# Optimization experiments

Hardware: AMD Instinct MI355X
Metric: run time of the kernel (lower is better)

Reference implementation:

```python
import jax, jax.numpy as jnp
import numpy as np
import math

B, S, D, H, L, V = 16, 512, 1024, 16, 128, 32000
DH = D // H


def _posenc(s, d):
    pos = np.arange(s, dtype=np.float32)[:, None]
    div = np.exp(np.arange(0, d, 2, dtype=np.float32) * (-math.log(10000.0) / d))
    pe = np.zeros((s, d), dtype=np.float32)
    pe[:, 0::2] = np.sin(pos * div)
    pe[:, 1::2] = np.cos(pos * div)
    return jnp.asarray(pe)


def _ln(x, g, b):
    m = jnp.mean(x, axis=-1, keepdims=True)
    v = jnp.mean((x - m) ** 2, axis=-1, keepdims=True)
    return (x - m) / jnp.sqrt(v + 1e-5) * g + b


def setup_inputs():
    key = jax.random.key(0)
    ks = jax.random.split(key, 16)
    w = lambda k, *sh: 0.02 * jax.random.normal(k, sh, dtype=jnp.float32)
    return {
        'x': jax.random.randint(ks[0], (B, S), 0, V),
        'embed': w(ks[1], V, D),
        'Wq': w(ks[2], D, D), 'bq': jnp.zeros((D,), jnp.float32),
        'Wk': w(ks[3], D, D), 'bk': jnp.zeros((D,), jnp.float32),
        'Wv': w(ks[4], D, D), 'bv': jnp.zeros((D,), jnp.float32),
        'Wo': w(ks[5], D, D), 'bo': jnp.zeros((D,), jnp.float32),
        'g1': jnp.ones((D,), jnp.float32), 'be1': jnp.zeros((D,), jnp.float32),
        'W1': w(ks[6], D, D), 'bf1': jnp.zeros((D,), jnp.float32),
        'W2': w(ks[7], D, D), 'bf2': jnp.zeros((D,), jnp.float32),
        'g2': jnp.ones((D,), jnp.float32), 'be2': jnp.zeros((D,), jnp.float32),
        'g3': jnp.ones((D,), jnp.float32), 'be3': jnp.zeros((D,), jnp.float32),
        'Wmu': w(ks[8], D, L), 'bmu': jnp.zeros((L,), jnp.float32),
        'Wsig': w(ks[9], D, L), 'bsig': jnp.zeros((L,), jnp.float32),
        'eps': jax.random.normal(ks[10], (B, S, L), dtype=jnp.float32),
    }


def reference(x, embed, Wq, bq, Wk, bk, Wv, bv, Wo, bo, g1, be1, W1, bf1, W2, bf2,
              g2, be2, g3, be3, Wmu, bmu, Wsig, bsig, eps):
    h = embed[x] * jnp.asarray(D ** 0.5, jnp.float32)          # [B,S,D]
    h = h + _posenc(S, D)                                       # dropout = identity (eval)
    h = _ln(h, g1, be1)
    # attention (faithful to source: raw reshape head-split, scale = dh/2)
    Q = (h @ Wq + bq).reshape(B, H, S, DH)
    K = (h @ Wk + bk).reshape(B, H, S, DH)
    Vv = (h @ Wv + bv).reshape(B, H, S, DH)
    scores = jnp.einsum('bhqd,bhkd->bhqk', Q, K) / (DH / 2.0)
    attn = jax.nn.softmax(scores, axis=-1)
    ctx = jnp.einsum('bhqk,bhkd->bhqd', attn, Vv).reshape(B, S, D)
    ctx = ctx @ Wo + bo
    h = h + ctx
    h = _ln(h, g2, be2)
    f = jax.nn.leaky_relu(h @ W1 + bf1, 0.01) @ W2 + bf2
    h = f + f                                                    # source: x = ffn(x); x = x + drop2(x)
    h = _ln(h, g3, be3)
    mu = h @ Wmu + bmu
    sigma = jnp.exp(h @ Wsig + bsig)
    z = mu + sigma * eps
    return z
```

## Files before the change

### kernel.cpp

```cpp
#include <hip/hip_runtime.h>
#include <cstdint>


typedef __bf16 bf16;
typedef __bf16 bf16x8 __attribute__((ext_vector_type(8)));
typedef __bf16 bf16x4 __attribute__((ext_vector_type(4)));
typedef float f32x4 __attribute__((ext_vector_type(4)));

#define MFMA16(a, b, c) __builtin_amdgcn_mfma_f32_16x16x32_bf16((a), (b), (c), 0, 0, 0)

#if __has_builtin(__builtin_amdgcn_exp2f)
#define EXP2F(x) __builtin_amdgcn_exp2f(x)
#else
#define EXP2F(x) exp2f(x)
#endif

__device__ __forceinline__ void async16(const bf16* g, bf16* l) {
  __builtin_amdgcn_global_load_lds(
      (const __attribute__((address_space(1))) unsigned int*)g,
      (__attribute__((address_space(3))) unsigned int*)l, 16, 0, 0);
}

#define VMWAIT(N)                                        \
  do {                                                   \
    asm volatile("s_waitcnt vmcnt(" #N ")" ::: "memory"); \
    __builtin_amdgcn_sched_barrier(0);                   \
  } while (0)
#define BAR() __builtin_amdgcn_s_barrier()

struct TP8 {
  const float* src[8];
  bf16* dst[8];
  int ncol[8];
};
__global__ __launch_bounds__(256) void transpose8_kernel(TP8 p) {
  const int z = blockIdx.z;
  const int N = p.ncol[z];
  const int tk = blockIdx.x * 64, tn = blockIdx.y * 64;
  if (tn >= N) return;
  const float* __restrict__ W = p.src[z];
  bf16* __restrict__ Wt = p.dst[z];
  __shared__ float tile[64][65];
  const int a = threadIdx.x >> 6, b = threadIdx.x & 63;
#pragma unroll
  for (int i = 0; i < 16; ++i) {
    int k = a + i * 4;
    tile[k][b] = W[(size_t)(tk + k) * N + tn + b];
  }
  __syncthreads();
#pragma unroll
  for (int i = 0; i < 16; ++i) {
    int n = a + i * 4;
    Wt[(size_t)(tn + n) * 1024 + tk + b] = (bf16)tile[b][n];
  }
}

__global__ __launch_bounds__(256) void embed_ln_kernel(const int* __restrict__ x,
                                                       const float* __restrict__ emb,
                                                       const float* __restrict__ g,
                                                       const float* __restrict__ be,
                                                       bf16* __restrict__ obf) {
  const int w = threadIdx.x >> 6, lane = threadIdx.x & 63;
  const int row = blockIdx.x * 4 + w;
  const int s = row & 511;
  const int t = x[row];
  const int c0 = lane * 16;
  const float* er = emb + (size_t)t * 1024 + c0;
  float o[16];
#pragma unroll
  for (int i = 0; i < 4; ++i) {
    const float4 e = *(const float4*)(er + i * 4);
    o[i * 4 + 0] = e.x; o[i * 4 + 1] = e.y; o[i * 4 + 2] = e.z; o[i * 4 + 3] = e.w;
  }
#pragma unroll
  for (int p = 0; p < 8; ++p) {
    const int cc = c0 + 2 * p;
    const float freq = __expf((float)cc * (-9.210340371976184f / 1024.0f));
    const float ang = (float)s * freq;
    o[2 * p] = o[2 * p] * 32.0f + __sinf(ang);
    o[2 * p + 1] = o[2 * p + 1] * 32.0f + __cosf(ang);
  }
  float sm = 0.f, q = 0.f;
#pragma unroll
  for (int j = 0; j < 16; ++j) { sm += o[j]; q += o[j] * o[j]; }
#pragma unroll
  for (int off = 1; off < 64; off <<= 1) {
    sm += __shfl_xor(sm, off);
    q += __shfl_xor(q, off);
  }
  const float mean = sm * (1.0f / 1024.0f);
  const float var = q * (1.0f / 1024.0f) - mean * mean;
  const float rstd = rsqrtf(var + 1e-5f);
  bf16 ob[16];
#pragma unroll
  for (int i = 0; i < 4; ++i) {
    const float4 gv = *(const float4*)(g + c0 + i * 4);
    const float4 bv = *(const float4*)(be + c0 + i * 4);
    const float gvv[4] = {gv.x, gv.y, gv.z, gv.w};
    const float bvv[4] = {bv.x, bv.y, bv.z, bv.w};
#pragma unroll
    for (int j = 0; j < 4; ++j)
      ob[i * 4 + j] = (bf16)((o[i * 4 + j] - mean) * rstd * gvv[j] + bvv[j]);
  }
  bf16* dst = obf + (size_t)row * 1024 + c0;
  *(uint4*)dst = *(const uint4*)&ob[0];
  *(uint4*)(dst + 8) = *(const uint4*)&ob[8];
}

__global__ __launch_bounds__(256) void ln_kernel(const bf16* __restrict__ in,
                                                 const float* __restrict__ g,
                                                 const float* __restrict__ be,
                                                 bf16* __restrict__ obf) {
  const int w = threadIdx.x >> 6, lane = threadIdx.x & 63;
  const int row = blockIdx.x * 4 + w;
  const int c0 = lane * 16;
  const bf16* src = in + (size_t)row * 1024 + c0;
  const bf16x8 v0 = *(const bf16x8*)src;
  const bf16x8 v1 = *(const bf16x8*)(src + 8);
  float v[16];
#pragma unroll
  for (int j = 0; j < 8; ++j) { v[j] = (float)v0[j]; v[8 + j] = (float)v1[j]; }
  float s = 0.f, q = 0.f;
#pragma unroll
  for (int j = 0; j < 16; ++j) { s += v[j]; q += v[j] * v[j]; }
#pragma unroll
  for (int off = 1; off < 64; off <<= 1) {
    s += __shfl_xor(s, off);
    q += __shfl_xor(q, off);
  }
  const float mean = s * (1.0f / 1024.0f);
  const float var = q * (1.0f / 1024.0f) - mean * mean;
  const float rstd = rsqrtf(var + 1e-5f);
  bf16 ob[16];
#pragma unroll
  for (int i = 0; i < 4; ++i) {
    const float4 gv = *(const float4*)(g + c0 + i * 4);
    const float4 bv = *(const float4*)(be + c0 + i * 4);
    const float gvv[4] = {gv.x, gv.y, gv.z, gv.w};
    const float bvv[4] = {bv.x, bv.y, bv.z, bv.w};
#pragma unroll
    for (int j = 0; j < 4; ++j)
      ob[i * 4 + j] = (bf16)((v[i * 4 + j] - mean) * rstd * gvv[j] + bvv[j]);
  }
  bf16* dst = obf + (size_t)row * 1024 + c0;
  *(uint4*)dst = *(const uint4*)&ob[0];
  *(uint4*)(dst + 8) = *(const uint4*)&ob[8];
}

__device__ __forceinline__ void ld_frags2(const bf16* sm, int rbase, int l15,
                                          int quad, bf16x8 out[2][2]) {
#pragma unroll
  for (int f = 0; f < 2; ++f) {
    const int row = rbase + f * 16 + l15;
    const int rx = row & 7;
#pragma unroll
    for (int h = 0; h < 2; ++h) {
      const int c = (h * 4 + quad) ^ rx;
      out[f][h] = *(const bf16x8*)(sm + (row * 8 + c) * 8);
    }
  }
}

template <int MQ, int NQ>
__device__ __forceinline__ void mma8(const bf16x8 aF[2][2], const bf16x8 bF[2][2],
                                     f32x4 acc[4][4]) {
  __builtin_amdgcn_s_setprio(1);
#pragma unroll
  for (int h = 0; h < 2; ++h)
#pragma unroll
    for (int m2 = 0; m2 < 2; ++m2)
#pragma unroll
      for (int n2 = 0; n2 < 2; ++n2)
        acc[MQ * 2 + m2][NQ * 2 + n2] =
            MFMA16(aF[m2][h], bF[n2][h], acc[MQ * 2 + m2][NQ * 2 + n2]);
  __builtin_amdgcn_s_setprio(0);
}

template <int MODE>
__global__ __launch_bounds__(512, 2) void gemm8_kernel(
    const bf16* __restrict__ A, const bf16* __restrict__ Bt,
    const float* __restrict__ b0f, const float* __restrict__ b1f,
    const float* __restrict__ b2f,
    bf16* __restrict__ o0, bf16* __restrict__ o1, bf16* __restrict__ o2,
    const bf16* __restrict__ residb,
    int M, int N, int K) {
  (void)M;
  __shared__ __attribute__((aligned(16))) bf16 Asm[2][128 * 64];
  __shared__ __attribute__((aligned(16))) bf16 Bsm[2][256 * 64];
  const int tid = threadIdx.x;
  const int wv = tid >> 6, lane = tid & 63;
  const int quad = lane >> 4, l15 = lane & 15;
  const int wm = wv & 1, wn = wv >> 1;
  const int m0 = blockIdx.x * 128, n0 = blockIdx.y * 256;

  f32x4 acc[4][4];
#pragma unroll
  for (int i = 0; i < 4; ++i)
#pragma unroll
    for (int j = 0; j < 4; ++j) acc[i][j] = {0.f, 0.f, 0.f, 0.f};

  size_t aoff[2], boff[2];
  int slds[2];
#pragma unroll
  for (int i = 0; i < 2; ++i) {
    const int s = tid + i * 512;
    const int r = s >> 3, c = (s & 7) ^ (r & 7);
    aoff[i] = (size_t)(m0 + r) * K + c * 8;
    boff[i] = (size_t)(n0 + r) * K + c * 8;
    slds[i] = s * 8;
  }
  auto stageA = [&](int buf, int t) {
#pragma unroll
    for (int i = 0; i < 2; ++i) async16(A + aoff[i] + t * 64, &Asm[buf][slds[i]]);
  };
  auto stageB = [&](int buf, int hh, int t) {
    const size_t ho = (size_t)hh * 128 * K;
    const int hl = hh * 8192;
#pragma unroll
    for (int i = 0; i < 2; ++i)
      async16(Bt + boff[i] + ho + t * 64, &Bsm[buf][hl + slds[i]]);
  };

  stageB(0, 0, 0); stageB(0, 1, 0); stageA(0, 0);
  stageB(1, 0, 1); stageB(1, 1, 1); stageA(1, 1);
  VMWAIT(6);
  BAR();

  bf16x8 aF[2][2], bF0[2][2], bF1[2][2];
  const int am0 = wm * 64, bn0 = wn * 64;

  auto phases = [&](int ne, int no, bool hn) {
    ld_frags2(&Asm[0][0], am0, l15, quad, aF);
    ld_frags2(&Bsm[0][0], bn0, l15, quad, bF0);
    BAR();
    mma8<0, 0>(aF, bF0, acc);
    BAR();
    ld_frags2(&Bsm[0][0], bn0 + 32, l15, quad, bF1);
    BAR();
    mma8<0, 1>(aF, bF1, acc);
    BAR();
    ld_frags2(&Asm[0][0], am0 + 32, l15, quad, aF);
    if (hn) stageB(0, 0, ne);
    BAR();
    mma8<1, 1>(aF, bF1, acc);
    BAR();
    if (hn) stageB(0, 1, ne);
    BAR();
    mma8<1, 0>(aF, bF0, acc);
    if (hn) { VMWAIT(4); } else { VMWAIT(0); }
    BAR();
    ld_frags2(&Asm[1][0], am0, l15, quad, aF);
    ld_frags2(&Bsm[1][0], bn0, l15, quad, bF0);
    if (hn) stageA(0, ne);
    BAR();
    mma8<0, 0>(aF, bF0, acc);
    BAR();
    ld_frags2(&Bsm[1][0], bn0 + 32, l15, quad, bF1);
    BAR();
    mma8<0, 1>(aF, bF1, acc);
    BAR();
    ld_frags2(&Asm[1][0], am0 + 32, l15, quad, aF);
    if (hn) stageB(1, 0, no);
    BAR();
    mma8<1, 1>(aF, bF1, acc);
    BAR();
    if (hn) { stageB(1, 1, no); stageA(1, no); }
    BAR();
    mma8<1, 0>(aF, bF0, acc);
    if (hn) { VMWAIT(6); }
    BAR();
  };

  const int nIter = K >> 7;
  for (int it = 0; it + 1 < nIter; ++it) phases(2 * it + 2, 2 * it + 3, true);
  phases(0, 0, false);

  const int part = (MODE == 6) ? ((int)blockIdx.y >> 2) : 0;
  bf16* ob = o0;
  const float* bp = b0f;
  if constexpr (MODE == 6) {
    ob = (part == 0) ? o0 : (part == 1 ? o1 : o2);
    bp = (part == 0) ? b0f : (part == 1 ? b1f : b2f);
  }
#pragma unroll
  for (int ni = 0; ni < 4; ++ni) {
    const int col = n0 + wn * 64 + ni * 16 + l15;
    const int cl = (MODE == 6) ? (col - part * 1024) : col;
    const float bv = bp[cl];
#pragma unroll
    for (int mi = 0; mi < 4; ++mi) {
#pragma unroll
      for (int r = 0; r < 4; ++r) {
        const int row = m0 + wm * 64 + mi * 16 + quad * 4 + r;
        float v = acc[mi][ni][r] + bv;
        if constexpr (MODE == 1) {
          const size_t idx = (size_t)row * N + col;
          o0[idx] = (bf16)(v + (float)residb[idx]);
        } else if constexpr (MODE == 2) {
          o0[(size_t)row * N + col] = (bf16)(v > 0.f ? v : 0.01f * v);
        } else if constexpr (MODE == 3) {
          o0[(size_t)row * N + col] = (bf16)(2.0f * v);
        } else {
          ob[(size_t)row * 1024 + cl] = (bf16)v;
        }
      }
    }
  }
}

__global__ __launch_bounds__(256) void gemm_musig(const bf16* __restrict__ A,
                                                  const bf16* __restrict__ Bt,
                                                  const float* __restrict__ bmu,
                                                  const float* __restrict__ bsig,
                                                  float* __restrict__ of) {
  constexpr int BK = 64;
  __shared__ __attribute__((aligned(16))) bf16 Asm[2][64 * BK];
  __shared__ __attribute__((aligned(16))) bf16 Bsm[2][128 * BK];
  const int tid = threadIdx.x;
  const int wv = tid >> 6, lane = tid & 63;
  const int quad = lane >> 4, l15 = lane & 15;
  const int m0 = blockIdx.x * 64, n0 = blockIdx.y * 128;
  const int wm = wv & 1, wn = wv >> 1;

  f32x4 acc[2][4];
#pragma unroll
  for (int i = 0; i < 2; ++i)
#pragma unroll
    for (int j = 0; j < 4; ++j) acc[i][j] = {0.f, 0.f, 0.f, 0.f};

  const bf16* Aglb[2];
  int asoff[2];
#pragma unroll
  for (int i = 0; i < 2; ++i) {
    const int s = tid + i * 256;
    const int row = s >> 3, col = (s & 7) ^ (row & 7);
    Aglb[i] = A + (size_t)(m0 + row) * 1024 + col * 8;
    asoff[i] = s * 8;
  }
  const bf16* Bglb[4];
  int bsoff[4];
#pragma unroll
  for (int i = 0; i < 4; ++i) {
    const int s = tid + i * 256;
    const int row = s >> 3, col = (s & 7) ^ (row & 7);
    Bglb[i] = Bt + (size_t)(n0 + row) * 1024 + col * 8;
    bsoff[i] = s * 8;
  }

#pragma unroll
  for (int i = 0; i < 2; ++i) async16(Aglb[i], &Asm[0][asoff[i]]);
#pragma unroll
  for (int i = 0; i < 4; ++i) async16(Bglb[i], &Bsm[0][bsoff[i]]);
  __syncthreads();

  for (int k = 0; k < 16; ++k) {
    const int cur = k & 1, nxt = cur ^ 1;
    bf16x8 af[2][2], bfr[4][2];
#pragma unroll
    for (int mi = 0; mi < 2; ++mi) {
      const int row = wm * 32 + mi * 16 + l15;
#pragma unroll
      for (int h = 0; h < 2; ++h) {
        const int pos = (h * 4 + quad) ^ (row & 7);
        af[mi][h] = *(const bf16x8*)(&Asm[cur][(row * 8 + pos) * 8]);
      }
    }
#pragma unroll
    for (int ni = 0; ni < 4; ++ni) {
      const int row = wn * 64 + ni * 16 + l15;
#pragma unroll
      for (int h = 0; h < 2; ++h) {
        const int pos = (h * 4 + quad) ^ (row & 7);
        bfr[ni][h] = *(const bf16x8*)(&Bsm[cur][(row * 8 + pos) * 8]);
      }
    }
    if (k + 1 < 16) {
      const int ko = (k + 1) * BK;
#pragma unroll
      for (int i = 0; i < 2; ++i) async16(Aglb[i] + ko, &Asm[nxt][asoff[i]]);
#pragma unroll
      for (int i = 0; i < 4; ++i) async16(Bglb[i] + ko, &Bsm[nxt][bsoff[i]]);
    }
#pragma unroll
    for (int h = 0; h < 2; ++h)
#pragma unroll
      for (int mi = 0; mi < 2; ++mi)
#pragma unroll
        for (int ni = 0; ni < 4; ++ni)
          acc[mi][ni] = MFMA16(af[mi][h], bfr[ni][h], acc[mi][ni]);
    __syncthreads();
  }

#pragma unroll
  for (int ni = 0; ni < 4; ++ni) {
    const int col = n0 + wn * 64 + ni * 16 + l15;
    const float bv = (col < 128) ? bmu[col] : bsig[col - 128];
#pragma unroll
    for (int mi = 0; mi < 2; ++mi) {
#pragma unroll
      for (int r = 0; r < 4; ++r) {
        const int row = m0 + wm * 32 + mi * 16 + quad * 4 + r;
        of[(size_t)row * 256 + col] = acc[mi][ni][r] + bv;
      }
    }
  }
}

__global__ __launch_bounds__(256) void vtrans_kernel(const bf16* __restrict__ Vb,
                                                     bf16* __restrict__ VtG) {
  __shared__ float t[64][65];
  const int bh = blockIdx.x, kt = blockIdx.y;
  const int tid = threadIdx.x;
  const bf16* src = Vb + (size_t)bh * 32768 + (size_t)kt * 4096;
#pragma unroll
  for (int i = 0; i < 2; ++i) {
    int s = i * 256 + tid;
    int r = s >> 3, c = (s & 7) * 8;
    bf16x8 v = *(const bf16x8*)(src + (size_t)s * 8);
#pragma unroll
    for (int j = 0; j < 8; ++j) t[r][c + j] = (float)v[j];
  }
  __syncthreads();
  bf16* dst = VtG + (size_t)bh * 32768 + kt * 64;
#pragma unroll
  for (int i = 0; i < 2; ++i) {
    int s = i * 256 + tid;
    int d = s >> 3, kc = (s & 7) * 8;
    bf16 tmp[8];
#pragma unroll
    for (int j = 0; j < 8; ++j) tmp[j] = (bf16)t[kc + j][d];
    *(uint4*)(dst + (size_t)d * 512 + kc) = *(const uint4*)tmp;
  }
}

__global__ __launch_bounds__(256) void attn_kernel(const bf16* __restrict__ Qg,
                                                   const bf16* __restrict__ Kg,
                                                   const bf16* __restrict__ Vt,
                                                   bf16* __restrict__ ctx) {
  __shared__ __attribute__((aligned(16))) bf16 Ksm[128 * 64];
  __shared__ __attribute__((aligned(16))) bf16 Vsm[64 * 128];
  __shared__ __attribute__((aligned(16))) bf16 Psm[4][16 * 128];
  const int tid = threadIdx.x;
  const int w = tid >> 6, lane = tid & 63;
  const int quad = lane >> 4, l15 = lane & 15;
  const int bh = blockIdx.x;
  const size_t base = (size_t)bh * 32768;
  const bf16* Vth = Vt + base;
  const int qbase = blockIdx.y * 128 + w * 32;
  const f32x4 fz = {0.f, 0.f, 0.f, 0.f};

  bf16x8 a[2][2];
#pragma unroll
  for (int qt = 0; qt < 2; ++qt)
#pragma unroll
    for (int hf = 0; hf < 2; ++hf) {
      bf16x8 tq = *(const bf16x8*)(Qg + base +
                   (size_t)(qbase + qt * 16 + l15) * 64 + hf * 32 + quad * 8);
#pragma unroll
      for (int e = 0; e < 8; ++e) tq[e] = (bf16)((float)tq[e] * 0.045111758f);
      a[qt][hf] = tq;
    }

  f32x4 o[2][4];
  float l_i[2][4];
#pragma unroll
  for (int qt = 0; qt < 2; ++qt)
#pragma unroll
    for (int i = 0; i < 4; ++i) { o[qt][i] = fz; l_i[qt][i] = 0.f; }

  for (int kv0 = 0; kv0 < 512; kv0 += 128) {
#pragma unroll
    for (int i = 0; i < 4; ++i) {
      int s = i * 256 + tid;
      int r = s >> 3, c = (s & 7) ^ (r & 7);
      async16(Kg + base + (size_t)(kv0 + r) * 64 + c * 8, &Ksm[s * 8]);
    }
#pragma unroll
    for (int i = 0; i < 4; ++i) {
      int s = i * 256 + tid;
      int d = s >> 4, cs = s & 15;
      int c = (cs & 8) | ((cs & 7) ^ (d & 7));
      async16(Vth + (size_t)d * 512 + kv0 + c * 8, &Vsm[s * 8]);
    }
    __syncthreads();

    f32x4 sc[2][8];
#pragma unroll
    for (int j = 0; j < 8; ++j) {
      const int n = j * 16 + l15;
      const bf16x8 k0 = *(const bf16x8*)(&Ksm[(n * 8 + (quad ^ (n & 7))) * 8]);
      const bf16x8 k1 = *(const bf16x8*)(&Ksm[(n * 8 + ((4 + quad) ^ (n & 7))) * 8]);
      sc[0][j] = MFMA16(a[0][0], k0, fz);
      sc[0][j] = MFMA16(a[0][1], k1, sc[0][j]);
      sc[1][j] = MFMA16(a[1][0], k0, fz);
      sc[1][j] = MFMA16(a[1][1], k1, sc[1][j]);
    }

    bf16* ps = &Psm[w][0];
#pragma unroll
    for (int qt = 0; qt < 2; ++qt) {
#pragma unroll
      for (int r = 0; r < 4; ++r) {
        const int prow = quad * 4 + r;
        float sum = 0.f;
#pragma unroll
        for (int j = 0; j < 8; ++j) {
          const float p = EXP2F(sc[qt][j][r]);
          sum += p;
          const int col = j * 16 + l15;
          const int cc = col >> 3;
          const int ccs = (cc & 8) | ((cc & 7) ^ (prow & 7));
          ps[prow * 128 + ccs * 8 + (col & 7)] = (bf16)p;
        }
        l_i[qt][r] += sum;
      }
#pragma unroll
      for (int c32 = 0; c32 < 4; ++c32) {
        const int pc = c32 * 4 + quad;
        const int pcs = (pc & 8) | ((pc & 7) ^ (l15 & 7));
        const bf16x8 pf = *(const bf16x8*)(ps + l15 * 128 + pcs * 8);
#pragma unroll
        for (int ni = 0; ni < 4; ++ni) {
          const int d = ni * 16 + l15;
          const int vcs = (pc & 8) | ((pc & 7) ^ (d & 7));
          const bf16x8 vf = *(const bf16x8*)(&Vsm[(d * 16 + vcs) * 8]);
          o[qt][ni] = MFMA16(pf, vf, o[qt][ni]);
        }
      }
    }
    __syncthreads();
  }

#pragma unroll
  for (int qt = 0; qt < 2; ++qt) {
#pragma unroll
    for (int r = 0; r < 4; ++r) {
      float l = l_i[qt][r];
      l += __shfl_xor(l, 1);
      l += __shfl_xor(l, 2);
      l += __shfl_xor(l, 4);
      l += __shfl_xor(l, 8);
      const float inv = 1.0f / l;
#pragma unroll
      for (int ni = 0; ni < 4; ++ni)
        ctx[base + (size_t)(qbase + qt * 16 + quad * 4 + r) * 64 + ni * 16 + l15]
            = (bf16)(o[qt][ni][r] * inv);
    }
  }
}

__global__ __launch_bounds__(256) void final_kernel(const float* __restrict__ musg,
                                                    const float* __restrict__ eps,
                                                    float* __restrict__ z) {
  const int i = blockIdx.x * 256 + threadIdx.x;
  const int row = i >> 5;
  const int c = (i & 31) * 4;
  const float4 m = *(const float4*)(musg + (size_t)row * 256 + c);
  const float4 s = *(const float4*)(musg + (size_t)row * 256 + 128 + c);
  const float4 e = *(const float4*)(eps + (size_t)row * 128 + c);
  float4 r;
  r.x = m.x + __expf(s.x) * e.x;
  r.y = m.y + __expf(s.y) * e.y;
  r.z = m.z + __expf(s.z) * e.z;
  r.w = m.w + __expf(s.w) * e.w;
  *(float4*)(z + (size_t)row * 128 + c) = r;
}

extern "C" void kernel_launch(void* const* d_in, const int* in_sizes, int n_in,
                              void* d_out, int out_size, void* d_ws, size_t ws_size,
                              hipStream_t stream) {
  (void)in_sizes; (void)n_in; (void)out_size; (void)ws_size;
  const int* x = (const int*)d_in[0];
  const float* emb = (const float*)d_in[1];
  const float* Wq = (const float*)d_in[2];
  const float* bq = (const float*)d_in[3];
  const float* Wk = (const float*)d_in[4];
  const float* bkb = (const float*)d_in[5];
  const float* Wv = (const float*)d_in[6];
  const float* bv = (const float*)d_in[7];
  const float* Wo = (const float*)d_in[8];
  const float* bo = (const float*)d_in[9];
  const float* g1 = (const float*)d_in[10];
  const float* be1 = (const float*)d_in[11];
  const float* W1 = (const float*)d_in[12];
  const float* bf1 = (const float*)d_in[13];
  const float* W2 = (const float*)d_in[14];
  const float* bf2 = (const float*)d_in[15];
  const float* g2 = (const float*)d_in[16];
  const float* be2 = (const float*)d_in[17];
  const float* g3 = (const float*)d_in[18];
  const float* be3 = (const float*)d_in[19];
  const float* Wmu = (const float*)d_in[20];
  const float* bmu = (const float*)d_in[21];
  const float* Wsig = (const float*)d_in[22];
  const float* bsig = (const float*)d_in[23];
  const float* eps = (const float*)d_in[24];
  float* z = (float*)d_out;

  const int M = 8192, D = 1024;
  char* ws = (char*)d_ws;
  size_t off = 0;
  auto alloc = [&](size_t b) {
    char* p = ws + off;
    off += (b + 255) & ~(size_t)255;
    return p;
  };
  bf16* wqkvT = (bf16*)alloc((size_t)3072 * 1024 * 2);
  bf16* woT = (bf16*)alloc((size_t)1024 * 1024 * 2);
  bf16* w1T = (bf16*)alloc((size_t)1024 * 1024 * 2);
  bf16* w2T = (bf16*)alloc((size_t)1024 * 1024 * 2);
  bf16* wmsT = (bf16*)alloc((size_t)256 * 1024 * 2);
  bf16* hb = (bf16*)alloc((size_t)M * D * 2);
  bf16* Qb = (bf16*)alloc((size_t)M * D * 2);
  bf16* Kb = (bf16*)alloc((size_t)M * D * 2);
  bf16* Vb = (bf16*)alloc((size_t)M * D * 2);
  bf16* VtG = (bf16*)alloc((size_t)M * D * 2);
  bf16* Cb = (bf16*)alloc((size_t)M * D * 2);
  bf16* h2b = (bf16*)alloc((size_t)M * D * 2);
  bf16* h3b = (bf16*)alloc((size_t)M * D * 2);
  bf16* hidb = (bf16*)alloc((size_t)M * D * 2);
  bf16* h4b = (bf16*)alloc((size_t)M * D * 2);
  bf16* h5b = (bf16*)alloc((size_t)M * D * 2);
  float* musg = (float*)alloc((size_t)M * 256 * 4);

  dim3 b256(256);
  dim3 b512(512);
  TP8 tp;
  tp.src[0] = Wq;   tp.dst[0] = wqkvT;                        tp.ncol[0] = 1024;
  tp.src[1] = Wk;   tp.dst[1] = wqkvT + (size_t)1024 * 1024;  tp.ncol[1] = 1024;
  tp.src[2] = Wv;   tp.dst[2] = wqkvT + (size_t)2048 * 1024;  tp.ncol[2] = 1024;
  tp.src[3] = Wo;   tp.dst[3] = woT;                          tp.ncol[3] = 1024;
  tp.src[4] = W1;   tp.dst[4] = w1T;                          tp.ncol[4] = 1024;
  tp.src[5] = W2;   tp.dst[5] = w2T;                          tp.ncol[5] = 1024;
  tp.src[6] = Wmu;  tp.dst[6] = wmsT;                         tp.ncol[6] = 128;
  tp.src[7] = Wsig; tp.dst[7] = wmsT + (size_t)128 * 1024;    tp.ncol[7] = 128;
  transpose8_kernel<<<dim3(16, 16, 8), b256, 0, stream>>>(tp);

  embed_ln_kernel<<<2048, b256, 0, stream>>>(x, emb, g1, be1, hb);

  gemm8_kernel<6><<<dim3(64, 12), b512, 0, stream>>>(hb, wqkvT, bq, bkb, bv,
                                                     Qb, Kb, Vb, nullptr,
                                                     M, 3072, D);
  vtrans_kernel<<<dim3(256, 8), b256, 0, stream>>>(Vb, VtG);
  attn_kernel<<<dim3(256, 4), b256, 0, stream>>>(Qb, Kb, VtG, Cb);

  gemm8_kernel<1><<<dim3(64, 4), b512, 0, stream>>>(Cb, woT, bo, nullptr, nullptr,
                                                    h2b, nullptr, nullptr, hb,
                                                    M, D, D);
  ln_kernel<<<2048, b256, 0, stream>>>(h2b, g2, be2, h3b);
  gemm8_kernel<2><<<dim3(64, 4), b512, 0, stream>>>(h3b, w1T, bf1, nullptr, nullptr,
                                                    hidb, nullptr, nullptr, nullptr,
                                                    M, D, D);
  gemm8_kernel<3><<<dim3(64, 4), b512, 0, stream>>>(hidb, w2T, bf2, nullptr, nullptr,
                                                    h4b, nullptr, nullptr, nullptr,
                                                    M, D, D);
  ln_kernel<<<2048, b256, 0, stream>>>(h4b, g3, be3, h5b);
  gemm_musig<<<dim3(128, 2), b256, 0, stream>>>(h5b, wmsT, bmu, bsig, musg);
  final_kernel<<<1024, b256, 0, stream>>>(musg, eps, z);
}
```

Baseline: 438.1 us.

## Fold LayerNorm affine into following GEMMs and fuse reparam epilogue

LayerNorm before W1 and before Wmu/Wsig is rewritten algebraically: gamma is folded into the transposed weights, and per-column sums of gamma*W and beta*W are precomputed. A small row-stats kernel now emits only rstd and -rstd*mean, which the GEMM epilogue applies to the raw accumulator. This avoids writing and re-reading the normalized activation tensors. The mu/sigma GEMM also absorbs the final exp/eps kernel, so one launch and the musig buffer disappear. The cost is an extra coefficient kernel, and the GEMMs now run on unnormalized bf16 inputs, which can lose precision when row means are large.

Result: slower. 508.1 us (+16.0%).

```diff
diff --git a/kernel.cpp b/kernel.cpp
--- a/kernel.cpp
+++ b/kernel.cpp
@@ -30,6 +30,7 @@
 
 struct TP8 {
   const float* src[8];
+  const float* gsrc[8];
   bf16* dst[8];
   int ncol[8];
 };
@@ -48,11 +49,42 @@
     tile[k][b] = W[(size_t)(tk + k) * N + tn + b];
   }
   __syncthreads();
+  const float* gsc = p.gsrc[z];
+  const float gv = gsc ? gsc[tk + b] : 1.0f;
 #pragma unroll
   for (int i = 0; i < 16; ++i) {
     int n = a + i * 4;
-    Wt[(size_t)(tn + n) * 1024 + tk + b] = (bf16)tile[b][n];
-  }
+    Wt[(size_t)(tn + n) * 1024 + tk + b] = (bf16)(tile[b][n] * gv);
+  }
+}
+
+struct LC3 {
+  const float* W[3];
+  const float* g[3];
+  const float* be[3];
+  float* c1[3];
+  float* c2[3];
+  int N[3];
+};
+__global__ __launch_bounds__(256) void lncoef_kernel(LC3 p) {
+  const int e = blockIdx.y;
+  const int N = p.N[e];
+  const int n = blockIdx.x * 256 + threadIdx.x;
+  if (n >= N) return;
+  const float* __restrict__ W = p.W[e];
+  const float* __restrict__ g = p.g[e];
+  const float* __restrict__ be = p.be[e];
+  float a1 = 0.f, a2 = 0.f;
+  for (int k = 0; k < 1024; k += 4) {
+#pragma unroll
+    for (int u = 0; u < 4; ++u) {
+      const float v = W[(size_t)(k + u) * N + n];
+      a1 += g[k + u] * v;
+      a2 += be[k + u] * v;
+    }
+  }
+  p.c1[e][n] = a1;
+  p.c2[e][n] = a2;
 }
 
 __global__ __launch_bounds__(256) void embed_ln_kernel(const int* __restrict__ x,
@@ -107,22 +139,22 @@
   *(uint4*)(dst + 8) = *(const uint4*)&ob[8];
 }
 
-__global__ __launch_bounds__(256) void ln_kernel(const bf16* __restrict__ in,
-                                                 const float* __restrict__ g,
-                                                 const float* __restrict__ be,
-                                                 bf16* __restrict__ obf) {
+__global__ __launch_bounds__(256) void rowstats_kernel(const bf16* __restrict__ in,
+                                                       float* __restrict__ rs,
+                                                       float* __restrict__ rm) {
   const int w = threadIdx.x >> 6, lane = threadIdx.x & 63;
   const int row = blockIdx.x * 4 + w;
   const int c0 = lane * 16;
   const bf16* src = in + (size_t)row * 1024 + c0;
   const bf16x8 v0 = *(const bf16x8*)src;
   const bf16x8 v1 = *(const bf16x8*)(src + 8);
-  float v[16];
-#pragma unroll
-  for (int j = 0; j < 8; ++j) { v[j] = (float)v0[j]; v[8 + j] = (float)v1[j]; }
   float s = 0.f, q = 0.f;
 #pragma unroll
-  for (int j = 0; j < 16; ++j) { s += v[j]; q += v[j] * v[j]; }
+  for (int j = 0; j < 8; ++j) {
+    const float a = (float)v0[j], b = (float)v1[j];
+    s += a + b;
+    q += a * a + b * b;
+  }
 #pragma unroll
   for (int off = 1; off < 64; off <<= 1) {
     s += __shfl_xor(s, off);
@@ -131,20 +163,10 @@
   const float mean = s * (1.0f / 1024.0f);
   const float var = q * (1.0f / 1024.0f) - mean * mean;
   const float rstd = rsqrtf(var + 1e-5f);
-  bf16 ob[16];
-#pragma unroll
-  for (int i = 0; i < 4; ++i) {
-    const float4 gv = *(const float4*)(g + c0 + i * 4);
-    const float4 bv = *(const float4*)(be + c0 + i * 4);
-    const float gvv[4] = {gv.x, gv.y, gv.z, gv.w};
-    const float bvv[4] = {bv.x, bv.y, bv.z, bv.w};
-#pragma unroll
-    for (int j = 0; j < 4; ++j)
-      ob[i * 4 + j] = (bf16)((v[i * 4 + j] - mean) * rstd * gvv[j] + bvv[j]);
-  }
-  bf16* dst = obf + (size_t)row * 1024 + c0;
-  *(uint4*)dst = *(const uint4*)&ob[0];
-  *(uint4*)(dst + 8) = *(const uint4*)&ob[8];
+  if (lane == 0) {
+    rs[row] = rstd;
+    rm[row] = -rstd * mean;
+  }
 }
 
 __device__ __forceinline__ void ld_frags2(const bf16* sm, int rbase, int l15,
@@ -183,6 +205,7 @@
     const float* __restrict__ b2f,
     bf16* __restrict__ o0, bf16* __restrict__ o1, bf16* __restrict__ o2,
     const bf16* __restrict__ residb,
+    const float* __restrict__ rsP, const float* __restrict__ rmP,
     int M, int N, int K) {
   (void)M;
   __shared__ __attribute__((aligned(16))) bf16 Asm[2][128 * 64];
@@ -287,40 +310,42 @@
     const int col = n0 + wn * 64 + ni * 16 + l15;
     const int cl = (MODE == 6) ? (col - part * 1024) : col;
     const float bv = bp[cl];
+    float c1v = 0.f, c2v = 0.f;
+    if constexpr (MODE == 4) { c1v = b1f[col]; c2v = b2f[col]; }
 #pragma unroll
     for (int mi = 0; mi < 4; ++mi) {
 #pragma unroll
       for (int r = 0; r < 4; ++r) {
         const int row = m0 + wm * 64 + mi * 16 + quad * 4 + r;
-        float v = acc[mi][ni][r] + bv;
+        const float a = acc[mi][ni][r];
         if constexpr (MODE == 1) {
           const size_t idx = (size_t)row * N + col;
-          o0[idx] = (bf16)(v + (float)residb[idx]);
-        } else if constexpr (MODE == 2) {
+          o0[idx] = (bf16)(a + bv + (float)residb[idx]);
+        } else if constexpr (MODE == 4) {
+          const float v = rsP[row] * a + rmP[row] * c1v + c2v + bv;
           o0[(size_t)row * N + col] = (bf16)(v > 0.f ? v : 0.01f * v);
         } else if constexpr (MODE == 3) {
-          o0[(size_t)row * N + col] = (bf16)(2.0f * v);
+          o0[(size_t)row * N + col] = (bf16)(2.0f * (a + bv));
         } else {
-          ob[(size_t)row * 1024 + cl] = (bf16)v;
+          ob[(size_t)row * 1024 + cl] = (bf16)(a + bv);
         }
       }
     }
   }
 }
 
-__global__ __launch_bounds__(256) void gemm_musig(const bf16* __restrict__ A,
-                                                  const bf16* __restrict__ Bt,
-                                                  const float* __restrict__ bmu,
-                                                  const float* __restrict__ bsig,
-                                                  float* __restrict__ of) {
-  constexpr int BK = 64;
-  __shared__ __attribute__((aligned(16))) bf16 Asm[2][64 * BK];
-  __shared__ __attribute__((aligned(16))) bf16 Bsm[2][128 * BK];
+__global__ __launch_bounds__(256) void gemm_musig_z(
+    const bf16* __restrict__ A, const bf16* __restrict__ Bt,
+    const float* __restrict__ rsP, const float* __restrict__ rmP,
+    const float* __restrict__ c1, const float* __restrict__ c2,
+    const float* __restrict__ bmu, const float* __restrict__ bsig,
+    const float* __restrict__ eps, float* __restrict__ z) {
+  __shared__ __attribute__((aligned(16))) bf16 Asm[2][32 * 64];
+  __shared__ __attribute__((aligned(16))) bf16 Bsm[2][256 * 64];
   const int tid = threadIdx.x;
   const int wv = tid >> 6, lane = tid & 63;
   const int quad = lane >> 4, l15 = lane & 15;
-  const int m0 = blockIdx.x * 64, n0 = blockIdx.y * 128;
-  const int wm = wv & 1, wn = wv >> 1;
+  const int m0 = blockIdx.x * 32;
 
   f32x4 acc[2][4];
 #pragma unroll
@@ -328,29 +353,27 @@
 #pragma unroll
     for (int j = 0; j < 4; ++j) acc[i][j] = {0.f, 0.f, 0.f, 0.f};
 
-  const bf16* Aglb[2];
-  int asoff[2];
-#pragma unroll
-  for (int i = 0; i < 2; ++i) {
+  const bf16* Ag;
+  int as_;
+  {
+    const int s = tid;
+    const int r = s >> 3, c = (s & 7) ^ (r & 7);
+    Ag = A + (size_t)(m0 + r) * 1024 + c * 8;
+    as_ = s * 8;
+  }
+  const bf16* Bg[8];
+  int bs_[8];
+#pragma unroll
+  for (int i = 0; i < 8; ++i) {
     const int s = tid + i * 256;
-    const int row = s >> 3, col = (s & 7) ^ (row & 7);
-    Aglb[i] = A + (size_t)(m0 + row) * 1024 + col * 8;
-    asoff[i] = s * 8;
-  }
-  const bf16* Bglb[4];
-  int bsoff[4];
-#pragma unroll
-  for (int i = 0; i < 4; ++i) {
-    const int s = tid + i * 256;
-    const int row = s >> 3, col = (s & 7) ^ (row & 7);
-    Bglb[i] = Bt + (size_t)(n0 + row) * 1024 + col * 8;
-    bsoff[i] = s * 8;
-  }
-
-#pragma unroll
-  for (int i = 0; i < 2; ++i) async16(Aglb[i], &Asm[0][asoff[i]]);
-#pragma unroll
-  for (int i = 0; i < 4; ++i) async16(Bglb[i], &Bsm[0][bsoff[i]]);
+    const int r = s >> 3, c = (s & 7) ^ (r & 7);
+    Bg[i] = Bt + (size_t)r * 1024 + c * 8;
+    bs_[i] = s * 8;
+  }
+
+  async16(Ag, &Asm[0][as_]);
+#pragma unroll
+  for (int i = 0; i < 8; ++i) async16(Bg[i], &Bsm[0][bs_[i]]);
   __syncthreads();
 
   for (int k = 0; k < 16; ++k) {
@@ -358,7 +381,7 @@
     bf16x8 af[2][2], bfr[4][2];
 #pragma unroll
     for (int mi = 0; mi < 2; ++mi) {
-      const int row = wm * 32 + mi * 16 + l15;
+      const int row = mi * 16 + l15;
 #pragma unroll
       for (int h = 0; h < 2; ++h) {
         const int pos = (h * 4 + quad) ^ (row & 7);
@@ -367,19 +390,18 @@
     }
 #pragma unroll
     for (int ni = 0; ni < 4; ++ni) {
-      const int row = wn * 64 + ni * 16 + l15;
+      const int nr = (ni < 2 ? wv * 32 + ni * 16 : 128 + wv * 32 + (ni - 2) * 16) + l15;
 #pragma unroll
       for (int h = 0; h < 2; ++h) {
-        const int pos = (h * 4 + quad) ^ (row & 7);
-        bfr[ni][h] = *(const bf16x8*)(&Bsm[cur][(row * 8 + pos) * 8]);
+        const int pos = (h * 4 + quad) ^ (nr & 7);
+        bfr[ni][h] = *(const bf16x8*)(&Bsm[cur][(nr * 8 + pos) * 8]);
       }
     }
     if (k + 1 < 16) {
-      const int ko = (k + 1) * BK;
-#pragma unroll
-      for (int i = 0; i < 2; ++i) async16(Aglb[i] + ko, &Asm[nxt][asoff[i]]);
-#pragma unroll
-      for (int i = 0; i < 4; ++i) async16(Bglb[i] + ko, &Bsm[nxt][bsoff[i]]);
+      const int ko = (k + 1) * 64;
+      async16(Ag + ko, &Asm[nxt][as_]);
+#pragma unroll
+      for (int i = 0; i < 8; ++i) async16(Bg[i] + ko, &Bsm[nxt][bs_[i]]);
     }
 #pragma unroll
     for (int h = 0; h < 2; ++h)
@@ -392,15 +414,18 @@
   }
 
 #pragma unroll
-  for (int ni = 0; ni < 4; ++ni) {
-    const int col = n0 + wn * 64 + ni * 16 + l15;
-    const float bv = (col < 128) ? bmu[col] : bsig[col - 128];
-#pragma unroll
-    for (int mi = 0; mi < 2; ++mi) {
-#pragma unroll
-      for (int r = 0; r < 4; ++r) {
-        const int row = m0 + wm * 32 + mi * 16 + quad * 4 + r;
-        of[(size_t)row * 256 + col] = acc[mi][ni][r] + bv;
+  for (int mi = 0; mi < 2; ++mi) {
+#pragma unroll
+    for (int r = 0; r < 4; ++r) {
+      const int row = m0 + mi * 16 + quad * 4 + r;
+      const float rs = rsP[row], rm = rmP[row];
+#pragma unroll
+      for (int cg = 0; cg < 2; ++cg) {
+        const int cmu = wv * 32 + cg * 16 + l15;
+        const int csg = 128 + cmu;
+        const float mu = rs * acc[mi][cg][r] + rm * c1[cmu] + c2[cmu] + bmu[cmu];
+        const float sg = rs * acc[mi][2 + cg][r] + rm * c1[csg] + c2[csg] + bsig[cmu];
+        z[(size_t)row * 128 + cmu] = mu + __expf(sg) * eps[(size_t)row * 128 + cmu];
       }
     }
   }
@@ -547,23 +572,6 @@
             = (bf16)(o[qt][ni][r] * inv);
     }
   }
-}
-
-__global__ __launch_bounds__(256) void final_kernel(const float* __restrict__ musg,
-                                                    const float* __restrict__ eps,
-                                                    float* __restrict__ z) {
-  const int i = blockIdx.x * 256 + threadIdx.x;
-  const int row = i >> 5;
-  const int c = (i & 31) * 4;
-  const float4 m = *(const float4*)(musg + (size_t)row * 256 + c);
-  const float4 s = *(const float4*)(musg + (size_t)row * 256 + 128 + c);
-  const float4 e = *(const float4*)(eps + (size_t)row * 128 + c);
-  float4 r;
-  r.x = m.x + __expf(s.x) * e.x;
-  r.y = m.y + __expf(s.y) * e.y;
-  r.z = m.z + __expf(s.z) * e.z;
-  r.w = m.w + __expf(s.w) * e.w;
-  *(float4*)(z + (size_t)row * 128 + c) = r;
 }
 
 extern "C" void kernel_launch(void* const* d_in, const int* in_sizes, int n_in,
@@ -617,44 +625,57 @@
   bf16* VtG = (bf16*)alloc((size_t)M * D * 2);
   bf16* Cb = (bf16*)alloc((size_t)M * D * 2);
   bf16* h2b = (bf16*)alloc((size_t)M * D * 2);
-  bf16* h3b = (bf16*)alloc((size_t)M * D * 2);
   bf16* hidb = (bf16*)alloc((size_t)M * D * 2);
   bf16* h4b = (bf16*)alloc((size_t)M * D * 2);
-  bf16* h5b = (bf16*)alloc((size_t)M * D * 2);
-  float* musg = (float*)alloc((size_t)M * 256 * 4);
+  float* rs2 = (float*)alloc((size_t)M * 4);
+  float* rm2 = (float*)alloc((size_t)M * 4);
+  float* rs3 = (float*)alloc((size_t)M * 4);
+  float* rm3 = (float*)alloc((size_t)M * 4);
+  float* c1w1 = (float*)alloc((size_t)1024 * 4);
+  float* c2w1 = (float*)alloc((size_t)1024 * 4);
+  float* c1ms = (float*)alloc((size_t)256 * 4);
+  float* c2ms = (float*)alloc((size_t)256 * 4);
 
   dim3 b256(256);
   dim3 b512(512);
   TP8 tp;
+  for (int i = 0; i < 8; ++i) tp.gsrc[i] = nullptr;
   tp.src[0] = Wq;   tp.dst[0] = wqkvT;                        tp.ncol[0] = 1024;
   tp.src[1] = Wk;   tp.dst[1] = wqkvT + (size_t)1024 * 1024;  tp.ncol[1] = 1024;
   tp.src[2] = Wv;   tp.dst[2] = wqkvT + (size_t)2048 * 1024;  tp.ncol[2] = 1024;
   tp.src[3] = Wo;   tp.dst[3] = woT;                          tp.ncol[3] = 1024;
-  tp.src[4] = W1;   tp.dst[4] = w1T;                          tp.ncol[4] = 1024;
+  tp.src[4] = W1;   tp.dst[4] = w1T;   tp.ncol[4] = 1024;     tp.gsrc[4] = g2;
   tp.src[5] = W2;   tp.dst[5] = w2T;                          tp.ncol[5] = 1024;
-  tp.src[6] = Wmu;  tp.dst[6] = wmsT;                         tp.ncol[6] = 128;
+  tp.src[6] = Wmu;  tp.dst[6] = wmsT;  tp.ncol[6] = 128;      tp.gsrc[6] = g3;
   tp.src[7] = Wsig; tp.dst[7] = wmsT + (size_t)128 * 1024;    tp.ncol[7] = 128;
+  tp.gsrc[7] = g3;
   transpose8_kernel<<<dim3(16, 16, 8), b256, 0, stream>>>(tp);
+
+  LC3 lc;
+  lc.W[0] = W1;   lc.g[0] = g2; lc.be[0] = be2; lc.c1[0] = c1w1;       lc.c2[0] = c2w1;       lc.N[0] = 1024;
+  lc.W[1] = Wmu;  lc.g[1] = g3; lc.be[1] = be3; lc.c1[1] = c1ms;       lc.c2[1] = c2ms;       lc.N[1] = 128;
+  lc.W[2] = Wsig; lc.g[2] = g3; lc.be[2] = be3; lc.c1[2] = c1ms + 128; lc.c2[2] = c2ms + 128; lc.N[2] = 128;
+  lncoef_kernel<<<dim3(4, 3), b256, 0, stream>>>(lc);
 
   embed_ln_kernel<<<2048, b256, 0, stream>>>(x, emb, g1, be1, hb);
 
   gemm8_kernel<6><<<dim3(64, 12), b512, 0, stream>>>(hb, wqkvT, bq, bkb, bv,
                                                      Qb, Kb, Vb, nullptr,
-                                                     M, 3072, D);
+                                                     nullptr, nullptr, M, 3072, D);
   vtrans_kernel<<<dim3(256, 8), b256, 0, stream>>>(Vb, VtG);
   attn_kernel<<<dim3(256, 4), b256, 0, stream>>>(Qb, Kb, VtG, Cb);
 
   gemm8_kernel<1><<<dim3(64, 4), b512, 0, stream>>>(Cb, woT, bo, nullptr, nullptr,
                                                     h2b, nullptr, nullptr, hb,
-                                                    M, D, D);
-  ln_kernel<<<2048, b256, 0, stream>>>(h2b, g2, be2, h3b);
-  gemm8_kernel<2><<<dim3(64, 4), b512, 0, stream>>>(h3b, w1T, bf1, nullptr, nullptr,
+                                                    nullptr, nullptr, M, D, D);
+  rowstats_kernel<<<2048, b256, 0, stream>>>(h2b, rs2, rm2);
+  gemm8_kernel<4><<<dim3(64, 4), b512, 0, stream>>>(h2b, w1T, bf1, c1w1, c2w1,
                                                     hidb, nullptr, nullptr, nullptr,
-                                                    M, D, D);
+                                                    rs2, rm2, M, D, D);
   gemm8_kernel<3><<<dim3(64, 4), b512, 0, stream>>>(hidb, w2T, bf2, nullptr, nullptr,
                                                     h4b, nullptr, nullptr, nullptr,
-                                                    M, D, D);
-  ln_kernel<<<2048, b256, 0, stream>>>(h4b, g3, be3, h5b);
-  gemm_musig<<<dim3(128, 2), b256, 0, stream>>>(h5b, wmsT, bmu, bsig, musg);
-  final_kernel<<<1024, b256, 0, stream>>>(musg, eps, z);
-}
+                                                    nullptr, nullptr, M, D, D);
+  rowstats_kernel<<<2048, b256, 0, stream>>>(h4b, rs3, rm3);
+  gemm_musig_z<<<dim3(256), b256, 0, stream>>>(h4b, wmsT, rs3, rm3, c1ms, c2ms,
+                                               bmu, bsig, eps, z);
+}
```
